# Optimization experiments

Hardware: AMD Instinct MI355X
Metric: run time of the kernel (lower is better)

## Reference

```python
import jax, jax.numpy as jnp
import numpy as np

S, B, H, Dh = 3072, 1, 16, 64

def setup_inputs() -> dict:
    key = jax.random.key(0)
    kq, kk, kv, km = jax.random.split(key, 4)
    query = jax.random.normal(kq, (S, B, H, Dh), dtype=jnp.float32)
    key_t = jax.random.normal(kk, (S, B, H, Dh), dtype=jnp.float32)
    value = jax.random.normal(kv, (S, B, H, Dh), dtype=jnp.float32)
    attention_mask = jax.random.randint(km, (1, 1, S, S), 0, 2).astype(bool)  # True = keep
    return {"query": query, "key": key_t, "value": value,
            "attention_mask": attention_mask, "attn_mask_type": 0}

def reference(query, key, value, attention_mask, attn_mask_type):
    # sbhd -> bshd
    q = jnp.transpose(query, (1, 0, 2, 3))   # (B,Sq,H,D)
    k = jnp.transpose(key,   (1, 0, 2, 3))   # (B,Sk,H,D)
    v = jnp.transpose(value, (1, 0, 2, 3))   # (B,Sk,H,D)
    scale = 1.0 / jnp.sqrt(jnp.asarray(q.shape[-1], q.dtype))
    scores = jnp.einsum('bqhd,bkhd->bhqk', q, k) * scale  # (B,H,Sq,Sk)
    scores = jnp.where(attention_mask, scores, -jnp.inf)  # bool mask, True=keep
    attn = jax.nn.softmax(scores, axis=-1)
    out = jnp.einsum('bhqk,bkhd->bqhd', attn, v)           # (B,Sq,H,D)
    return out
```

## Files before the change

### kernel.cpp

```cpp
#include <hip/hip_runtime.h>
#include <stdint.h>

#define SEQ 3072
#define NH  16
#define DH  64
#define WQ  32
#define KVBLK 64
#define NKT (SEQ / KVBLK)
#define HALF_T (NKT / 2)
#define NQT (SEQ / WQ)
#define NWORDS (SEQ * SEQ / 64)

typedef __attribute__((ext_vector_type(8))) __bf16 bf16x8;
typedef __attribute__((ext_vector_type(16))) float f32x16;

union BF8 { ushort us[8]; uint u[4]; uint4 u4; bf16x8 v; };

__device__ __forceinline__ ushort f2bf(float f) {
    uint u = __builtin_bit_cast(uint, f);
    return (ushort)((u + 0x7FFFu + ((u >> 16) & 1u)) >> 16);
}

__global__ void detect_kernel(const uint32_t* __restrict__ m, int* __restrict__ flag) {
    __shared__ int cntA, cntB;
    if (threadIdx.x == 0) { cntA = 0; cntB = 0; }
    __syncthreads();
    int a = 0, b = 0;
    for (int i = 0; i < 16; ++i) {
        uint32_t w = m[threadIdx.x + i * 256];
        if (w & 0xFFFFFF00u) a = 1;
        if (w & 0x0000FFFFu) b = 1;
    }
    if (a) atomicOr(&cntA, 1);
    if (b) atomicOr(&cntB, 1);
    __syncthreads();
    if (threadIdx.x == 0) *flag = (cntA == 0) ? 1 : ((cntB == 0) ? 2 : 0);
}

#define SCALE_Q (0.125f * 1.44269504f)

__global__ __launch_bounds__(256)
void fused_prep(const float* __restrict__ K, const float* __restrict__ V,
                const float* __restrict__ Q, const void* __restrict__ mask,
                const int* __restrict__ flag,
                ushort* __restrict__ Kbz, ushort* __restrict__ Vtz,
                ushort* __restrict__ Qb, uint64_t* __restrict__ bits)
{
    const int b = blockIdx.x;
    const int tid = threadIdx.x;

    if (b < 768) {
        const int kt = b % NKT, h = b / NKT;
        __shared__ float Vf[64][68];
        {
            const int kr = tid >> 2, dc = (tid & 3) * 16;
            const float* vsrc = V + (((size_t)(kt * KVBLK + kr) * NH + h) * DH + dc);
            #pragma unroll
            for (int j = 0; j < 4; ++j) {
                float4 t = *(const float4*)(vsrc + 4 * j);
                Vf[kr][dc + 4 * j + 0] = t.x; Vf[kr][dc + 4 * j + 1] = t.y;
                Vf[kr][dc + 4 * j + 2] = t.z; Vf[kr][dc + 4 * j + 3] = t.w;
            }
        }

        ushort* kout = Kbz + ((size_t)(h * NKT + kt)) * 4096;
        #pragma unroll
        for (int i = 0; i < 2; ++i) {
            const int idx = tid + 256 * i;
            const int f = idx >> 6, l = idx & 63;
            const int kc = f >> 1, kh = f & 1;
            const int row = kh * 32 + (l & 31);
            const int kcol = kc * 16 + (l >> 5) * 8;
            const float* ks = K + (((size_t)(kt * KVBLK + row) * NH + h) * DH + kcol);
            float4 a = *(const float4*)(ks);
            float4 c = *(const float4*)(ks + 4);
            BF8 t;
            t.us[0] = f2bf(a.x); t.us[1] = f2bf(a.y); t.us[2] = f2bf(a.z); t.us[3] = f2bf(a.w);
            t.us[4] = f2bf(c.x); t.us[5] = f2bf(c.y); t.us[6] = f2bf(c.z); t.us[7] = f2bf(c.w);
            *(uint4*)(kout + idx * 8) = t.u4;
        }

        __syncthreads();

        ushort* vout = Vtz + ((size_t)(h * NKT + kt)) * 4096;
        #pragma unroll
        for (int i = 0; i < 2; ++i) {
            const int idx = tid + 256 * i;
            const int f = idx >> 6, l = idx & 63;
            const int kc = f >> 1, dh = f & 1;
            const int d = dh * 32 + (l & 31);
            const int kr0 = kc * 16 + (l >> 5) * 8;
            BF8 t;
            #pragma unroll
            for (int j = 0; j < 8; ++j)
                t.us[j] = f2bf(Vf[kr0 + j][d]);
            *(uint4*)(vout + idx * 8) = t.u4;
        }
    } else if (b < 1024) {
        for (int vb = b - 768; vb < SEQ * NH * DH / (256 * 8); vb += 256) {
            int i = (vb * 256 + tid) * 8;
            float4 a = *(const float4*)(Q + i);
            float4 c = *(const float4*)(Q + i + 4);
            BF8 t;
            t.us[0] = f2bf(a.x * SCALE_Q); t.us[1] = f2bf(a.y * SCALE_Q);
            t.us[2] = f2bf(a.z * SCALE_Q); t.us[3] = f2bf(a.w * SCALE_Q);
            t.us[4] = f2bf(c.x * SCALE_Q); t.us[5] = f2bf(c.y * SCALE_Q);
            t.us[6] = f2bf(c.z * SCALE_Q); t.us[7] = f2bf(c.w * SCALE_Q);
            *(uint4*)(Qb + i) = t.u4;
        }
    } else {
        const int f = *flag;
        for (int vb = b - 1024; vb < SEQ * SEQ / 256; vb += 1024) {
            const int g = vb * 256 + tid;
            bool v;
            if (f == 1)      v = ((const int*)mask)[g] != 0;
            else if (f == 2) v = ((const float*)mask)[g] != 0.0f;
            else             v = ((const unsigned char*)mask)[g] != 0;
            uint64_t bl = __ballot(v);
            if ((tid & 63) == 0) {
                int w = g >> 6;
                int qrow = w / NKT, cw = w % NKT;
                bits[(size_t)cw * SEQ + qrow] = bl;
            }
        }
    }
}

__device__ __forceinline__ bf16x8 ldfrag(const ushort* tile, int f, int lane) {
    return *(const bf16x8*)(tile + f * 512 + lane * 8);
}

__device__ __forceinline__ void process_tile(
    const bf16x8 kf[8], const bf16x8 vf[8], const bf16x8 qf[4],
    uint64_t mw, int hh, f32x16& o0, f32x16& o1, float& l_)
{
    const uint64_t mu = mw >> (4 * hh);
    const uint mlo = (uint)mu, mhi = (uint)(mu >> 32);
    f32x16 s0, s1;
    #pragma unroll
    for (int r = 0; r < 16; ++r) {
        const int sh = (r & 3) + 8 * (r >> 2);
        const uint b0 = (mlo >> sh) & 1u;
        const uint b1 = (mhi >> sh) & 1u;
        s0[r] = __builtin_bit_cast(float, (b0 - 1u) & 0xFF800000u);
        s1[r] = __builtin_bit_cast(float, (b1 - 1u) & 0xFF800000u);
    }

    __builtin_amdgcn_s_setprio(1);
    #pragma unroll
    for (int kc = 0; kc < 4; ++kc) {
        s0 = __builtin_amdgcn_mfma_f32_32x32x16_bf16(kf[kc * 2 + 0], qf[kc], s0, 0, 0, 0);
        s1 = __builtin_amdgcn_mfma_f32_32x32x16_bf16(kf[kc * 2 + 1], qf[kc], s1, 0, 0, 0);
    }
    __builtin_amdgcn_s_setprio(0);

    float la0 = 0.f, la1 = 0.f;
    #pragma unroll
    for (int r = 0; r < 16; ++r) {
        float p0 = __builtin_amdgcn_exp2f(s0[r]);
        float p1 = __builtin_amdgcn_exp2f(s1[r]);
        s0[r] = p0; s1[r] = p1;
        la0 += p0; la1 += p1;
    }
    l_ += la0 + la1;

    bf16x8 pa[4];
    {
        #define PKSWAP(dlo, dhi, a0, a1, b0, b1)                                   \
            {   uint wl, wh;                                                       \
                asm("v_cvt_pk_bf16_f32 %0, %1, %2" : "=v"(wl) : "v"(a0), "v"(a1)); \
                asm("v_cvt_pk_bf16_f32 %0, %1, %2" : "=v"(wh) : "v"(b0), "v"(b1)); \
                asm("v_permlane32_swap_b32 %0, %1" : "+v"(wl), "+v"(wh));          \
                dlo = wl; dhi = wh; }
        BF8 t0, t1, t2, t3;
        PKSWAP(t0.u[0], t0.u[2], s0[0],  s0[1],  s0[4],  s0[5]);
        PKSWAP(t0.u[1], t0.u[3], s0[2],  s0[3],  s0[6],  s0[7]);
        PKSWAP(t1.u[0], t1.u[2], s0[8],  s0[9],  s0[12], s0[13]);
        PKSWAP(t1.u[1], t1.u[3], s0[10], s0[11], s0[14], s0[15]);
        PKSWAP(t2.u[0], t2.u[2], s1[0],  s1[1],  s1[4],  s1[5]);
        PKSWAP(t2.u[1], t2.u[3], s1[2],  s1[3],  s1[6],  s1[7]);
        PKSWAP(t3.u[0], t3.u[2], s1[8],  s1[9],  s1[12], s1[13]);
        PKSWAP(t3.u[1], t3.u[3], s1[10], s1[11], s1[14], s1[15]);
        pa[0] = t0.v; pa[1] = t1.v; pa[2] = t2.v; pa[3] = t3.v;
        #undef PKSWAP
    }

    __builtin_amdgcn_s_setprio(1);
    #pragma unroll
    for (int kc = 0; kc < 4; ++kc) {
        o0 = __builtin_amdgcn_mfma_f32_32x32x16_bf16(pa[kc], vf[kc * 2 + 0], o0, 0, 0, 0);
        o1 = __builtin_amdgcn_mfma_f32_32x32x16_bf16(pa[kc], vf[kc * 2 + 1], o1, 0, 0, 0);
    }
    __builtin_amdgcn_s_setprio(0);
}

__global__ __launch_bounds__(256, 3)
void attn17(const ushort* __restrict__ Qb, const ushort* __restrict__ Kbz,
            const ushort* __restrict__ Vtz, const uint64_t* __restrict__ bits2,
            float* __restrict__ out)
{
    const int bid = blockIdx.x;
    const int swz = (bid & 7) * 96 + (bid >> 3);
    const int h = swz / 48, qg = swz % 48;
    const int tid = threadIdx.x;
    const int wv = tid >> 6, lane = tid & 63;
    const int qsub = wv & 1, kvh = wv >> 1;
    const int lq = lane & 31, hh = lane >> 5;
    const int qrow0 = (qg * 2 + qsub) * WQ;

    __shared__ __align__(16) float MergeF[2][2368];

    bf16x8 qf[4];
    {
        const ushort* qp = Qb + ((size_t)(qrow0 + lq) * NH + h) * DH;
        #pragma unroll
        for (int kc = 0; kc < 4; ++kc)
            qf[kc] = *(const bf16x8*)(qp + kc * 16 + hh * 8);
    }

    f32x16 o0, o1;
    #pragma unroll
    for (int i = 0; i < 16; ++i) { o0[i] = 0.f; o1[i] = 0.f; }
    float l_ = 0.f;

    const int kt0 = kvh * HALF_T;
    const ushort* kbase = Kbz + ((size_t)(h * NKT + kt0)) * 4096;
    const ushort* vbase = Vtz + ((size_t)(h * NKT + kt0)) * 4096;
    const uint64_t* bb = bits2 + (size_t)kt0 * SEQ + qrow0 + lq;

    for (int it = 0; it < HALF_T; ++it) {
        const ushort* kt_ = kbase + (size_t)it * 4096;
        const ushort* vt_ = vbase + (size_t)it * 4096;
        bf16x8 kA[8], vC[8];
        #pragma unroll
        for (int f = 0; f < 8; ++f) kA[f] = ldfrag(kt_, f, lane);
        #pragma unroll
        for (int f = 0; f < 8; ++f) vC[f] = ldfrag(vt_, f, lane);
        const uint64_t mw = bb[(size_t)it * SEQ];
        process_tile(kA, vC, qf, mw, hh, o0, o1, l_);
    }

    {
        float a = l_, b = l_;
        asm("v_permlane32_swap_b32 %0, %1" : "+v"(a), "+v"(b));
        l_ = a + b;
    }

    float* LMq = &MergeF[qsub][0];
    if (kvh == 1) {
        if (hh == 0) LMq[64 * 36 + lq] = l_;
        #pragma unroll
        for (int j = 0; j < 4; ++j) {
            float4 t0, t1;
            t0.x = o0[4 * j]; t0.y = o0[4 * j + 1]; t0.z = o0[4 * j + 2]; t0.w = o0[4 * j + 3];
            t1.x = o1[4 * j]; t1.y = o1[4 * j + 1]; t1.z = o1[4 * j + 2]; t1.w = o1[4 * j + 3];
            *(float4*)&LMq[lq * 36 + 4 * hh + 8 * j]        = t0;
            *(float4*)&LMq[(lq + 32) * 36 + 4 * hh + 8 * j] = t1;
        }
    }
    __syncthreads();
    if (kvh == 0) {
        const float lB = LMq[64 * 36 + lq];
        const float l = l_ + lB;
        const float inv = (l > 0.f) ? 1.0f / l : 0.f;
        #pragma unroll
        for (int r = 0; r < 16; ++r) {
            const int q_r = (r & 3) + 8 * (r >> 2) + 4 * hh;
            const float ir = __shfl(inv, q_r);
            float* op = out + ((size_t)(qrow0 + q_r) * NH + h) * DH;
            op[lq]      = (o0[r] + LMq[lq * 36 + q_r]) * ir;
            op[lq + 32] = (o1[r] + LMq[(lq + 32) * 36 + q_r]) * ir;
        }
    }
}

__global__ __launch_bounds__(256, 2)
void attn_fb(const float* __restrict__ Q, const float* __restrict__ K,
             const float* __restrict__ V, const int* __restrict__ mask_i32,
             float* __restrict__ out)
{
    const int qtile = blockIdx.x, h = blockIdx.y;
    const int tid  = threadIdx.x;
    const int wv   = tid >> 6, lane = tid & 63;
    const int g    = lane >> 4, c = lane & 15;
    const int qb   = qtile * 64 + wv * 16;

    typedef __attribute__((ext_vector_type(4))) float f32x4;
    __shared__ __align__(16) ushort KbS[KVBLK * 72];
    __shared__ __align__(16) ushort VtS[DH * 72];
    __shared__ __align__(16) ushort PbS[4 * 16 * 72];
    ushort* Pw = &PbS[wv * 16 * 72];

    bf16x8 qa[2];
    {
        const float* qp = Q + ((qb + c) * NH + h) * DH;
        #pragma unroll
        for (int kk = 0; kk < 2; ++kk) {
            BF8 t;
            const float4* pp = (const float4*)(qp + kk * 32 + g * 8);
            float4 f0 = pp[0], f1 = pp[1];
            t.us[0] = f2bf(f0.x * 0.125f); t.us[1] = f2bf(f0.y * 0.125f);
            t.us[2] = f2bf(f0.z * 0.125f); t.us[3] = f2bf(f0.w * 0.125f);
            t.us[4] = f2bf(f1.x * 0.125f); t.us[5] = f2bf(f1.y * 0.125f);
            t.us[6] = f2bf(f1.z * 0.125f); t.us[7] = f2bf(f1.w * 0.125f);
            qa[kk] = t.v;
        }
    }

    f32x4 oacc[4];
    float m_[4], lsum[4];
    #pragma unroll
    for (int nt = 0; nt < 4; ++nt) oacc[nt] = (f32x4){0.f, 0.f, 0.f, 0.f};
    #pragma unroll
    for (int r = 0; r < 4; ++r) { m_[r] = -1e30f; lsum[r] = 0.f; }

    const int srow0 = tid >> 3;
    const int fch   = tid & 7;

    for (int kt = 0; kt < NKT; ++kt) {
        __syncthreads();
        #pragma unroll
        for (int i = 0; i < 2; ++i) {
            const int krow = srow0 + 32 * i;
            const int gofs = ((kt * KVBLK + krow) * NH + h) * DH + fch * 8;
            const float4* kp = (const float4*)(K + gofs);
            const float4* vp = (const float4*)(V + gofs);
            float4 k0 = kp[0], k1 = kp[1];
            float4 v0 = vp[0], v1 = vp[1];
            BF8 kb;
            kb.us[0] = f2bf(k0.x); kb.us[1] = f2bf(k0.y);
            kb.us[2] = f2bf(k0.z); kb.us[3] = f2bf(k0.w);
            kb.us[4] = f2bf(k1.x); kb.us[5] = f2bf(k1.y);
            kb.us[6] = f2bf(k1.z); kb.us[7] = f2bf(k1.w);
            *(uint4*)&KbS[krow * 72 + (fch ^ (krow & 7)) * 8] = kb.u4;
            float vf[8] = {v0.x, v0.y, v0.z, v0.w, v1.x, v1.y, v1.z, v1.w};
            #pragma unroll
            for (int j = 0; j < 8; ++j) {
                const int d = fch * 8 + j;
                VtS[d * 72 + ((krow >> 3) ^ ((d >> 3) & 7)) * 8 + (krow & 7)] = f2bf(vf[j]);
            }
        }
        __syncthreads();

        f32x4 sacc[4];
        #pragma unroll
        for (int nt = 0; nt < 4; ++nt) sacc[nt] = (f32x4){0.f, 0.f, 0.f, 0.f};
        #pragma unroll
        for (int kk = 0; kk < 2; ++kk) {
            #pragma unroll
            for (int nt = 0; nt < 4; ++nt) {
                const int krow = nt * 16 + c;
                bf16x8 kf = *(const bf16x8*)&KbS[krow * 72 + (((g + 4 * kk) ^ (krow & 7))) * 8];
                sacc[nt] = __builtin_amdgcn_mfma_f32_16x16x32_bf16(qa[kk], kf, sacc[nt], 0, 0, 0);
            }
        }

        float pmax[4];
        #pragma unroll
        for (int r = 0; r < 4; ++r) pmax[r] = -1e30f;
        #pragma unroll
        for (int nt = 0; nt < 4; ++nt) {
            #pragma unroll
            for (int r = 0; r < 4; ++r) {
                bool keep = mask_i32[(size_t)(qb + 4 * g + r) * SEQ + kt * KVBLK + nt * 16 + c] != 0;
                float s = keep ? sacc[nt][r] : -1e30f;
                sacc[nt][r] = s;
                pmax[r] = fmaxf(pmax[r], s);
            }
        }
        #pragma unroll
        for (int r = 0; r < 4; ++r) {
            float v = pmax[r];
            v = fmaxf(v, __shfl_xor(v, 1));
            v = fmaxf(v, __shfl_xor(v, 2));
            v = fmaxf(v, __shfl_xor(v, 4));
            v = fmaxf(v, __shfl_xor(v, 8));
            float nm = fmaxf(m_[r], v);
            float alpha = __expf(m_[r] - nm);
            m_[r] = nm;
            lsum[r] *= alpha;
            #pragma unroll
            for (int nt = 0; nt < 4; ++nt) oacc[nt][r] *= alpha;
        }
        #pragma unroll
        for (int nt = 0; nt < 4; ++nt) {
            #pragma unroll
            for (int r = 0; r < 4; ++r) {
                float pv = __expf(sacc[nt][r] - m_[r]);
                lsum[r] += pv;
                const int row = 4 * g + r, col = nt * 16 + c;
                Pw[row * 72 + (((col >> 3) ^ (row & 7))) * 8 + (col & 7)] = f2bf(pv);
            }
        }
        #pragma unroll
        for (int kk = 0; kk < 2; ++kk) {
            bf16x8 pa = *(const bf16x8*)&Pw[c * 72 + (((g + 4 * kk) ^ (c & 7))) * 8];
            #pragma unroll
            for (int nt = 0; nt < 4; ++nt) {
                const int d = nt * 16 + c;
                bf16x8 vb = *(const bf16x8*)&VtS[d * 72 + (((g + 4 * kk) ^ ((d >> 3) & 7))) * 8];
                oacc[nt] = __builtin_amdgcn_mfma_f32_16x16x32_bf16(pa, vb, oacc[nt], 0, 0, 0);
            }
        }
    }

    #pragma unroll
    for (int r = 0; r < 4; ++r) {
        float v = lsum[r];
        v += __shfl_xor(v, 1); v += __shfl_xor(v, 2);
        v += __shfl_xor(v, 4); v += __shfl_xor(v, 8);
        lsum[r] = (v > 0.f) ? 1.0f / v : 0.f;
    }
    #pragma unroll
    for (int nt = 0; nt < 4; ++nt) {
        #pragma unroll
        for (int r = 0; r < 4; ++r) {
            out[((qb + 4 * g + r) * NH + h) * DH + nt * 16 + c] = oacc[nt][r] * lsum[r];
        }
    }
}

extern "C" void kernel_launch(void* const* d_in, const int* in_sizes, int n_in,
                              void* d_out, int out_size, void* d_ws, size_t ws_size,
                              hipStream_t stream) {
    const float* Q    = (const float*)d_in[0];
    const float* K    = (const float*)d_in[1];
    const float* V    = (const float*)d_in[2];
    const void*  mask = d_in[3];
    float* out = (float*)d_out;

    const size_t off_bits = 64;
    const size_t off_qb   = off_bits + (size_t)NWORDS * 8;
    const size_t off_kbz  = off_qb  + (size_t)SEQ * NH * DH * 2;
    const size_t off_vtz  = off_kbz + (size_t)SEQ * NH * DH * 2;
    const size_t need     = off_vtz + (size_t)SEQ * NH * DH * 2;

    if (ws_size >= need) {
        int*      flag = (int*)d_ws;
        uint64_t* bits = (uint64_t*)((char*)d_ws + off_bits);
        ushort*   Qb   = (ushort*)((char*)d_ws + off_qb);
        ushort*   Kbz  = (ushort*)((char*)d_ws + off_kbz);
        ushort*   Vtz  = (ushort*)((char*)d_ws + off_vtz);
        detect_kernel<<<1, 256, 0, stream>>>((const uint32_t*)mask, flag);
        fused_prep<<<2048, 256, 0, stream>>>(K, V, Q, mask, flag, Kbz, Vtz, Qb, bits);
        attn17<<<NQT * NH / 2, 256, 0, stream>>>(Qb, Kbz, Vtz, bits, out);
    } else {
        attn_fb<<<dim3(NKT, NH), 256, 0, stream>>>(Q, K, V, (const int*)mask, out);
    }
}
```

Before: 94.40 us.

## Software-pipeline QK and softmax-PV phases across alternating KV tiles

Splits per-tile processing into a QK phase and a softmax+PV phase, then ping-pongs two score buffers so the next tile's QK MFMAs are issued before the current tile's exp/PV work. The aim is to overlap MFMA with transcendental and pack work and to hide K/V load latency. The extra live accumulators raise register pressure, so launch bounds drop from 3 to 2 waves per SIMD, which lowers occupancy. On the last iteration the lookahead recomputes the final tile redundantly.

Result: no change. 95.52 us (+1.2%).

```diff
diff --git a/kernel.cpp b/kernel.cpp
--- a/kernel.cpp
+++ b/kernel.cpp
@@ -130,20 +130,21 @@
     return *(const bf16x8*)(tile + f * 512 + lane * 8);
 }
 
-__device__ __forceinline__ void process_tile(
-    const bf16x8 kf[8], const bf16x8 vf[8], const bf16x8 qf[4],
-    uint64_t mw, int hh, f32x16& o0, f32x16& o1, float& l_)
+__device__ __forceinline__ void qk_phase(
+    const ushort* ktile, int lane, const bf16x8 qf[4],
+    uint64_t mw, int hh, f32x16& s0, f32x16& s1)
 {
+    bf16x8 kf[8];
+    #pragma unroll
+    for (int f = 0; f < 8; ++f) kf[f] = ldfrag(ktile, f, lane);
+
     const uint64_t mu = mw >> (4 * hh);
     const uint mlo = (uint)mu, mhi = (uint)(mu >> 32);
-    f32x16 s0, s1;
     #pragma unroll
     for (int r = 0; r < 16; ++r) {
         const int sh = (r & 3) + 8 * (r >> 2);
-        const uint b0 = (mlo >> sh) & 1u;
-        const uint b1 = (mhi >> sh) & 1u;
-        s0[r] = __builtin_bit_cast(float, (b0 - 1u) & 0xFF800000u);
-        s1[r] = __builtin_bit_cast(float, (b1 - 1u) & 0xFF800000u);
+        s0[r] = __builtin_bit_cast(float, (((mlo >> sh) & 1u) - 1u) & 0xFF800000u);
+        s1[r] = __builtin_bit_cast(float, (((mhi >> sh) & 1u) - 1u) & 0xFF800000u);
     }
 
     __builtin_amdgcn_s_setprio(1);
@@ -153,6 +154,15 @@
         s1 = __builtin_amdgcn_mfma_f32_32x32x16_bf16(kf[kc * 2 + 1], qf[kc], s1, 0, 0, 0);
     }
     __builtin_amdgcn_s_setprio(0);
+}
+
+__device__ __forceinline__ void sm_pv_phase(
+    const ushort* vtile, int lane,
+    f32x16& s0, f32x16& s1, f32x16& o0, f32x16& o1, float& l_)
+{
+    bf16x8 vf[8];
+    #pragma unroll
+    for (int f = 0; f < 8; ++f) vf[f] = ldfrag(vtile, f, lane);
 
     float la0 = 0.f, la1 = 0.f;
     #pragma unroll
@@ -194,8 +204,8 @@
     __builtin_amdgcn_s_setprio(0);
 }
 
-__global__ __launch_bounds__(256, 3)
-void attn17(const ushort* __restrict__ Qb, const ushort* __restrict__ Kbz,
+__global__ __launch_bounds__(256, 2)
+void attn18(const ushort* __restrict__ Qb, const ushort* __restrict__ Kbz,
             const ushort* __restrict__ Vtz, const uint64_t* __restrict__ bits2,
             float* __restrict__ out)
 {
@@ -228,16 +238,19 @@
     const ushort* vbase = Vtz + ((size_t)(h * NKT + kt0)) * 4096;
     const uint64_t* bb = bits2 + (size_t)kt0 * SEQ + qrow0 + lq;
 
-    for (int it = 0; it < HALF_T; ++it) {
-        const ushort* kt_ = kbase + (size_t)it * 4096;
-        const ushort* vt_ = vbase + (size_t)it * 4096;
-        bf16x8 kA[8], vC[8];
-        #pragma unroll
-        for (int f = 0; f < 8; ++f) kA[f] = ldfrag(kt_, f, lane);
-        #pragma unroll
-        for (int f = 0; f < 8; ++f) vC[f] = ldfrag(vt_, f, lane);
-        const uint64_t mw = bb[(size_t)it * SEQ];
-        process_tile(kA, vC, qf, mw, hh, o0, o1, l_);
+    f32x16 sE0, sE1, sO0, sO1;
+
+    qk_phase(kbase, lane, qf, bb[0], hh, sE0, sE1);
+
+    for (int it = 0; it < HALF_T; it += 2) {
+        qk_phase(kbase + (size_t)(it + 1) * 4096, lane, qf,
+                 bb[(size_t)(it + 1) * SEQ], hh, sO0, sO1);
+        sm_pv_phase(vbase + (size_t)it * 4096, lane, sE0, sE1, o0, o1, l_);
+
+        const int t2 = (it + 2 < HALF_T) ? it + 2 : HALF_T - 1;
+        qk_phase(kbase + (size_t)t2 * 4096, lane, qf,
+                 bb[(size_t)t2 * SEQ], hh, sE0, sE1);
+        sm_pv_phase(vbase + (size_t)(it + 1) * 4096, lane, sO0, sO1, o0, o1, l_);
     }
 
     {
@@ -443,7 +456,7 @@
         ushort*   Vtz  = (ushort*)((char*)d_ws + off_vtz);
         detect_kernel<<<1, 256, 0, stream>>>((const uint32_t*)mask, flag);
         fused_prep<<<2048, 256, 0, stream>>>(K, V, Q, mask, flag, Kbz, Vtz, Qb, bits);
-        attn17<<<NQT * NH / 2, 256, 0, stream>>>(Qb, Kbz, Vtz, bits, out);
+        attn18<<<NQT * NH / 2, 256, 0, stream>>>(Qb, Kbz, Vtz, bits, out);
     } else {
         attn_fb<<<dim3(NKT, NH), 256, 0, stream>>>(Q, K, V, (const int*)mask, out);
     }
```
